# Performance work log

Measured on AMD Instinct MI355X. Metric: run time of the kernel, lower is better.

Reference implementation:

```python
import jax, jax.numpy as jnp
import numpy as np

H = 256  # rnn_size


def setup_inputs() -> dict:
    key = jax.random.key(0)
    ks = jax.random.split(key, 6)
    B, T, F, D = 64, 512, 64, 64
    s_in = 1.0 / np.sqrt(F)
    s_rec = 1.0 / np.sqrt(H)
    return {
        "x": jax.random.normal(ks[0], (B, T, F), jnp.float32),
        "kernel": jax.random.normal(ks[1], (F, 3 * H), jnp.float32) * s_in,
        "recurrent_kernel": jax.random.normal(ks[2], (H, 3 * H), jnp.float32) * s_rec,
        "bias": jax.random.normal(ks[3], (3 * H,), jnp.float32) * 0.01,
        "dense_w": jax.random.normal(ks[4], (H, D), jnp.float32) * s_rec,
        "dense_b": jax.random.normal(ks[5], (D,), jnp.float32) * 0.01,
    }


def _gru_scan(x, kernel, recurrent_kernel, bias):
    B, T, _ = x.shape
    # Pre-project all timesteps: [B, T, 3H]
    xproj = jnp.einsum("btf,fg->btg", x, kernel) + bias
    xproj_t = jnp.transpose(xproj, (1, 0, 2))  # [T, B, 3H]

    def step(h, xt):
        # Keras GRU, reset_after=False: r gates the recurrent matmul of the candidate
        rec = h @ recurrent_kernel  # [B, 3H]
        xz, xr, xh = xt[:, :H], xt[:, H:2 * H], xt[:, 2 * H:]
        rz, rr, rh = rec[:, :H], rec[:, H:2 * H], rec[:, 2 * H:]
        z = jax.nn.sigmoid(xz + rz)
        r = jax.nn.sigmoid(xr + rr)
        hh = jnp.tanh(xh + r * rh)
        h_new = z * h + (1.0 - z) * hh
        return h_new, h_new

    h0 = jnp.zeros((B, H), x.dtype)
    h_last, outs = jax.lax.scan(step, h0, xproj_t)
    return jnp.transpose(outs, (1, 0, 2)), h_last  # [B,T,H], [B,H]


def reference(x, kernel, recurrent_kernel, bias, dense_w, dense_b):
    outputs, h_last = _gru_scan(x, kernel, recurrent_kernel, bias)
    state = jnp.tanh(h_last @ dense_w + dense_b)  # [B, dense_size]
    return outputs, state
```

## Files before the change

### kernel.cpp

```cpp
#include <hip/hip_runtime.h>


typedef _Float16 half2_t __attribute__((ext_vector_type(2)));
typedef _Float16 f16x4_t __attribute__((ext_vector_type(4)));
typedef _Float16 f16x8_t __attribute__((ext_vector_type(8)));
typedef float f32x4_t __attribute__((ext_vector_type(4)));

#define LOG2E 1.4426950408889634f

__device__ __forceinline__ float fast_sigmoid(float x) {
  float e = __builtin_amdgcn_exp2f(-x * LOG2E);
  return __builtin_amdgcn_rcpf(1.0f + e);
}
__device__ __forceinline__ float fast_tanh(float x) {
  float e = __builtin_amdgcn_exp2f(x * (2.0f * LOG2E));
  return 1.0f - 2.0f * __builtin_amdgcn_rcpf(1.0f + e);
}

__global__ __launch_bounds__(256, 4) void xproj_gemm(
    const float* __restrict__ x, const float* __restrict__ kmat,
    const float* __restrict__ bias, _Float16* __restrict__ xp) {
  __shared__ half2_t As2[32][132];
  __shared__ half2_t Bs2[32][132];
  const int tid = threadIdx.x;
  const int rb = blockIdx.x * 128;
  const int cb = blockIdx.y * 128;

  {
    const int k4 = (tid & 15) * 4;
    const int r0 = tid >> 4;
#pragma unroll
    for (int p = 0; p < 8; ++p) {
      int r = r0 + p * 16;
      float4 v = *(const float4*)(x + (size_t)(rb + r) * 64 + k4);
      half2_t lo, hi;
      lo[0] = (_Float16)v.x; lo[1] = (_Float16)v.y;
      hi[0] = (_Float16)v.z; hi[1] = (_Float16)v.w;
      As2[k4 / 2][r] = lo;
      As2[k4 / 2 + 1][r] = hi;
    }
  }
  {
    const int c4 = (tid & 31) * 4;
    const int kp0 = tid >> 5;
#pragma unroll
    for (int p = 0; p < 4; ++p) {
      int kp = kp0 + p * 8;
      float4 va = *(const float4*)(kmat + (size_t)(2 * kp) * 768 + cb + c4);
      float4 vb = *(const float4*)(kmat + (size_t)(2 * kp + 1) * 768 + cb + c4);
      half2_t o0, o1, o2, o3;
      o0[0] = (_Float16)va.x; o0[1] = (_Float16)vb.x;
      o1[0] = (_Float16)va.y; o1[1] = (_Float16)vb.y;
      o2[0] = (_Float16)va.z; o2[1] = (_Float16)vb.z;
      o3[0] = (_Float16)va.w; o3[1] = (_Float16)vb.w;
      Bs2[kp][c4 + 0] = o0;
      Bs2[kp][c4 + 1] = o1;
      Bs2[kp][c4 + 2] = o2;
      Bs2[kp][c4 + 3] = o3;
    }
  }
  __syncthreads();

  const int tx = tid & 15, ty = tid >> 4;
  const int r0 = ty * 8;
  const int c0 = tx * 4;
  float acc[8][8];
  {
    float4 b0 = *(const float4*)(bias + cb + c0);
    float4 b1 = *(const float4*)(bias + cb + 64 + c0);
    float bz[8] = {b0.x, b0.y, b0.z, b0.w, b1.x, b1.y, b1.z, b1.w};
#pragma unroll
    for (int i = 0; i < 8; ++i)
#pragma unroll
      for (int j = 0; j < 8; ++j) acc[i][j] = bz[j];
  }

#pragma unroll 2
  for (int kp = 0; kp < 32; ++kp) {
    half2_t a2[8], b2[8];
    *(int4*)(&a2[0]) = *(const int4*)(&As2[kp][r0]);
    *(int4*)(&a2[4]) = *(const int4*)(&As2[kp][r0 + 4]);
    *(int2*)(&b2[0]) = *(const int2*)(&Bs2[kp][c0]);
    *(int2*)(&b2[2]) = *(const int2*)(&Bs2[kp][c0 + 2]);
    *(int2*)(&b2[4]) = *(const int2*)(&Bs2[kp][64 + c0]);
    *(int2*)(&b2[6]) = *(const int2*)(&Bs2[kp][64 + c0 + 2]);
#pragma unroll
    for (int i = 0; i < 8; ++i)
#pragma unroll
      for (int j = 0; j < 8; ++j)
        acc[i][j] = __builtin_amdgcn_fdot2(a2[i], b2[j], acc[i][j], false);
  }

#pragma unroll
  for (int i = 0; i < 8; ++i) {
    f16x4_t o0, o1;
#pragma unroll
    for (int j = 0; j < 4; ++j) {
      o0[j] = (_Float16)acc[i][j];
      o1[j] = (_Float16)acc[i][4 + j];
    }
    _Float16* dst = xp + (size_t)(rb + r0 + i) * 768 + cb;
    *(f16x4_t*)(dst + c0) = o0;
    *(f16x4_t*)(dst + 64 + c0) = o1;
  }
}

__global__ __launch_bounds__(512, 2) void gru_scan_mfma(
    const _Float16* __restrict__ xp, const float* __restrict__ wr,
    const float* __restrict__ dw, const float* __restrict__ db,
    float* __restrict__ out, float* __restrict__ state) {
  __shared__ alignas(16) _Float16 hA[2][256];

  const int tid = threadIdx.x;
  const int b = blockIdx.x;
  const int w = tid >> 6;
  const int l = tid & 63;
  const int q = l >> 4;
  const int nl = l & 15;

  f16x8_t wfrag[6][8];
#pragma unroll
  for (int i = 0; i < 6; ++i) {
    const int nt = w + 8 * i;
#pragma unroll
    for (int kt = 0; kt < 8; ++kt) {
      f16x8_t f;
#pragma unroll
      for (int j = 0; j < 8; ++j)
        f[j] = (_Float16)wr[(size_t)(kt * 32 + q * 8 + j) * 768 + nt * 16 + nl];
      wfrag[i][kt] = f;
    }
  }

  if (tid < 256) {
    hA[0][tid] = (_Float16)0.0f;
    hA[1][tid] = (_Float16)0.0f;
  }
  __syncthreads();

  const _Float16* xpb = xp + (size_t)b * 512 * 768;
  float* outb = out + (size_t)b * 512 * 256;
  const int col0 = w * 16 + nl;
  const int col1 = col0 + 128;
  float hold0 = 0.0f, hold1 = 0.0f;

  for (int t = 0; t < 512; ++t) {
    const int cur = t & 1;

    const _Float16* xrow = xpb + (size_t)t * 768;
    _Float16 xz0 = xrow[col0], xr0 = xrow[col0 + 256], xh0 = xrow[col0 + 512];
    _Float16 xz1 = xrow[col1], xr1 = xrow[col1 + 256], xh1 = xrow[col1 + 512];

    f32x4_t acc[6];
#pragma unroll
    for (int i = 0; i < 6; ++i) acc[i] = (f32x4_t){0.f, 0.f, 0.f, 0.f};
#pragma unroll
    for (int kt = 0; kt < 8; ++kt) {
      f16x8_t afrag = *(const f16x8_t*)&hA[cur][kt * 32 + q * 8];
#pragma unroll
      for (int i = 0; i < 6; ++i)
        acc[i] = __builtin_amdgcn_mfma_f32_16x16x32_f16(afrag, wfrag[i][kt],
                                                        acc[i], 0, 0, 0);
    }

    float z0 = fast_sigmoid((float)xz0 + acc[0][0]);
    float r0 = fast_sigmoid((float)xr0 + acc[2][0]);
    float hc0 = fast_tanh((float)xh0 + r0 * acc[4][0]);
    float hn0 = z0 * hold0 + (1.0f - z0) * hc0;
    hold0 = hn0;

    float z1 = fast_sigmoid((float)xz1 + acc[1][0]);
    float r1 = fast_sigmoid((float)xr1 + acc[3][0]);
    float hc1 = fast_tanh((float)xh1 + r1 * acc[5][0]);
    float hn1 = z1 * hold1 + (1.0f - z1) * hc1;
    hold1 = hn1;

    if (q == 0) {
      outb[(size_t)t * 256 + col0] = hn0;
      outb[(size_t)t * 256 + col1] = hn1;
      hA[1 - cur][col0] = (_Float16)hn0;
      hA[1 - cur][col1] = (_Float16)hn1;
    }
    __syncthreads();
  }

  if (tid < 64) {
    float acc = db[tid];
#pragma unroll 8
    for (int k = 0; k < 256; ++k)
      acc = fmaf((float)hA[0][k], dw[k * 64 + tid], acc);
    state[(size_t)b * 64 + tid] = fast_tanh(acc);
  }
}

extern "C" void kernel_launch(void* const* d_in, const int* in_sizes, int n_in,
                              void* d_out, int out_size, void* d_ws,
                              size_t ws_size, hipStream_t stream) {
  const float* x = (const float*)d_in[0];
  const float* kmat = (const float*)d_in[1];
  const float* wr = (const float*)d_in[2];
  const float* bias = (const float*)d_in[3];
  const float* dw = (const float*)d_in[4];
  const float* db = (const float*)d_in[5];

  float* out = (float*)d_out;
  float* state = out + (size_t)64 * 512 * 256;
  _Float16* xp = (_Float16*)d_ws;

  dim3 gg(32768 / 128, 768 / 128);
  xproj_gemm<<<gg, 256, 0, stream>>>(x, kmat, bias, xp);
  gru_scan_mfma<<<64, 512, 0, stream>>>(xp, wr, dw, db, out, state);
}
```

Measured before the change: 697.2 us.

## Prefetch xproj two steps ahead and use LDS-only barrier in GRU scan

Loads the precomputed input projections for timestep t+2 into registers during step t, double-buffered across two register sets, so global-memory latency leaves the serial recurrence critical path. Replaces __syncthreads with an inline s_waitcnt lgkmcnt(0) plus s_barrier, so the barrier no longer waits on the outstanding global loads and stores. This is safe only because the LDS writes are the sole cross-thread dependency. It adds registers per thread and relies on hand-written asm ordering.

```diff
diff --git a/kernel.cpp b/kernel.cpp
--- a/kernel.cpp
+++ b/kernel.cpp
@@ -15,6 +15,10 @@
 __device__ __forceinline__ float fast_tanh(float x) {
   float e = __builtin_amdgcn_exp2f(x * (2.0f * LOG2E));
   return 1.0f - 2.0f * __builtin_amdgcn_rcpf(1.0f + e);
+}
+
+__device__ __forceinline__ void sync_lds() {
+  asm volatile("s_waitcnt lgkmcnt(0)\n\ts_barrier" ::: "memory");
 }
 
 __global__ __launch_bounds__(256, 4) void xproj_gemm(
@@ -144,12 +148,18 @@
   const int col1 = col0 + 128;
   float hold0 = 0.0f, hold1 = 0.0f;
 
-  for (int t = 0; t < 512; ++t) {
+  _Float16 xva[6], xvb[6];
+  {
+    const _Float16* x0 = xpb;
+    const _Float16* x1 = xpb + 768;
+    xva[0] = x0[col0]; xva[1] = x0[col0 + 256]; xva[2] = x0[col0 + 512];
+    xva[3] = x0[col1]; xva[4] = x0[col1 + 256]; xva[5] = x0[col1 + 512];
+    xvb[0] = x1[col0]; xvb[1] = x1[col0 + 256]; xvb[2] = x1[col0 + 512];
+    xvb[3] = x1[col1]; xvb[4] = x1[col1 + 256]; xvb[5] = x1[col1 + 512];
+  }
+
+  auto step = [&](int t, _Float16* xv) {
     const int cur = t & 1;
-
-    const _Float16* xrow = xpb + (size_t)t * 768;
-    _Float16 xz0 = xrow[col0], xr0 = xrow[col0 + 256], xh0 = xrow[col0 + 512];
-    _Float16 xz1 = xrow[col1], xr1 = xrow[col1 + 256], xh1 = xrow[col1 + 512];
 
     f32x4_t acc[6];
 #pragma unroll
@@ -163,15 +173,15 @@
                                                         acc[i], 0, 0, 0);
     }
 
-    float z0 = fast_sigmoid((float)xz0 + acc[0][0]);
-    float r0 = fast_sigmoid((float)xr0 + acc[2][0]);
-    float hc0 = fast_tanh((float)xh0 + r0 * acc[4][0]);
+    float z0 = fast_sigmoid((float)xv[0] + acc[0][0]);
+    float r0 = fast_sigmoid((float)xv[1] + acc[2][0]);
+    float hc0 = fast_tanh((float)xv[2] + r0 * acc[4][0]);
     float hn0 = z0 * hold0 + (1.0f - z0) * hc0;
     hold0 = hn0;
 
-    float z1 = fast_sigmoid((float)xz1 + acc[1][0]);
-    float r1 = fast_sigmoid((float)xr1 + acc[3][0]);
-    float hc1 = fast_tanh((float)xh1 + r1 * acc[5][0]);
+    float z1 = fast_sigmoid((float)xv[3] + acc[1][0]);
+    float r1 = fast_sigmoid((float)xv[4] + acc[3][0]);
+    float hc1 = fast_tanh((float)xv[5] + r1 * acc[5][0]);
     float hn1 = z1 * hold1 + (1.0f - z1) * hc1;
     hold1 = hn1;
 
@@ -181,7 +191,18 @@
       hA[1 - cur][col0] = (_Float16)hn0;
       hA[1 - cur][col1] = (_Float16)hn1;
     }
-    __syncthreads();
+
+    int tp = t + 2 <= 511 ? t + 2 : 511;
+    const _Float16* xn = xpb + (size_t)tp * 768;
+    xv[0] = xn[col0]; xv[1] = xn[col0 + 256]; xv[2] = xn[col0 + 512];
+    xv[3] = xn[col1]; xv[4] = xn[col1 + 256]; xv[5] = xn[col1 + 512];
+
+    sync_lds();
+  };
+
+  for (int tt = 0; tt < 256; ++tt) {
+    step(2 * tt, xva);
+    step(2 * tt + 1, xvb);
   }
 
   if (tid < 64) {
```

Result: faster. 665.5 us (-4.5%).
